# Optimization experiments

Measured on AMD Instinct MI355X. Metric: run time of the kernel, lower is better.

Reference implementation:

```python
import jax, jax.numpy as jnp
import numpy as np

N_EMBED = 1024
HEAD_SIZE = 128
B, T = 4, 4096

def setup_inputs() -> dict:
    key = jax.random.key(0)
    kx, kk, kq, kv = jax.random.split(key, 4)
    s = (1.0 / np.sqrt(N_EMBED)).astype(np.float32)
    return {
        "x": jax.random.normal(kx, (B, T, N_EMBED), dtype=jnp.float32),
        "W_key": jax.random.normal(kk, (N_EMBED, HEAD_SIZE), dtype=jnp.float32) * s,
        "W_query": jax.random.normal(kq, (N_EMBED, HEAD_SIZE), dtype=jnp.float32) * s,
        "W_value": jax.random.normal(kv, (N_EMBED, HEAD_SIZE), dtype=jnp.float32) * s,
    }

def reference(x, W_key, W_query, W_value):
    # x: [B,T,C]; single-head causal attention. NOTE: scale is C**-0.5 (n_embed),
    # matching the original source (not head_size**-0.5).
    Bn, Tn, C = x.shape
    k = jnp.einsum('btc,cd->btd', x, W_key)    # [B,T,d]
    q = jnp.einsum('btc,cd->btd', x, W_query)  # [B,T,d]
    v = jnp.einsum('btc,cd->btd', x, W_value)  # [B,T,d]
    scores = jnp.einsum('btd,bsd->bts', q, k) * (C ** -0.5)  # [B,T,T]
    causal = jnp.tril(jnp.ones((Tn, Tn), dtype=bool))
    scores = jnp.where(causal[None, :, :], scores, -jnp.inf)
    attn = jax.nn.softmax(scores, axis=-1)
    return jnp.einsum('bts,bsd->btd', attn, v)
```

## Files before the change

### kernel.cpp

```cpp
#include <hip/hip_runtime.h>
#include <hip/hip_bf16.h>

typedef __attribute__((ext_vector_type(8))) short bf16x8;
typedef __attribute__((ext_vector_type(4))) float f32x4;
typedef __attribute__((ext_vector_type(4))) unsigned short us4;

__device__ __forceinline__ unsigned short f2bf(float f) {
    union { float f; unsigned u; } c; c.f = f;
    unsigned u = c.u;
    u += 0x7fffu + ((u >> 16) & 1u);
    return (unsigned short)(u >> 16);
}
__device__ __forceinline__ float bf2f(unsigned short h) {
    union { unsigned u; float f; } c; c.u = ((unsigned)h) << 16;
    return c.f;
}
__device__ __forceinline__ unsigned cvt_pk_bf16(float lo, float hi) {
    unsigned r;
    asm volatile("v_cvt_pk_bf16_f32 %0, %1, %2" : "=v"(r) : "v"(lo), "v"(hi));
    return r;
}

#define QSCALE 0.04508422f

__global__ __launch_bounds__(256) void wconv_kernel(
        const float* __restrict__ Wk, const float* __restrict__ Wq,
        const float* __restrict__ Wv, unsigned short* __restrict__ WbT) {
    int idx = blockIdx.x * 256 + threadIdx.x;
    int n = idx >> 10, kk = idx & 1023;
    const float* W = (n < 128) ? Wk : (n < 256) ? Wq : Wv;
    int col = n & 127;
    WbT[idx] = f2bf(W[kk * 128 + col]);
}

__global__ __launch_bounds__(512) void qkv_gemm_kernel(
        const float* __restrict__ x, const unsigned short* __restrict__ WbT,
        unsigned short* __restrict__ kw, unsigned short* __restrict__ qw,
        unsigned short* __restrict__ vTw) {
    __shared__ __align__(16) unsigned short Al[32 * 72];
    __shared__ __align__(16) unsigned short Bl[384 * 72];
    const int tid = threadIdx.x;
    const int m0 = blockIdx.x * 32;
    const int w = tid >> 6, l = tid & 63;
    const int l15 = l & 15, lh = l >> 4;
    const int wr = w >> 2, wc = w & 3;

    f32x4 acc[6] = {};

    const int ar = tid >> 4, ac = (tid & 15) * 4;

    float4 aV;
    bf16x8 bV[6];

    auto issue = [&](int k0) {
        aV = *(const float4*)&x[(size_t)(m0 + ar) * 1024 + k0 + ac];
        for (int it = 0; it < 6; ++it) {
            int idx = it * 512 + tid;
            bV[it] = *(const bf16x8*)&WbT[(size_t)(idx >> 3) * 1024 + k0 + (idx & 7) * 8];
        }
    };

    issue(0);
    for (int t = 0; t < 16; ++t) {
        {
            uint2 p;
            p.x = cvt_pk_bf16(aV.x, aV.y);
            p.y = cvt_pk_bf16(aV.z, aV.w);
            *(uint2*)&Al[ar * 72 + ac] = p;
        }
        for (int it = 0; it < 6; ++it) {
            int idx = it * 512 + tid;
            *(bf16x8*)&Bl[(idx >> 3) * 72 + (idx & 7) * 8] = bV[it];
        }
        __syncthreads();
        if (t + 1 < 16) issue((t + 1) * 64);
        for (int kc = 0; kc < 2; ++kc) {
            bf16x8 a = *(bf16x8*)&Al[(wr * 16 + l15) * 72 + kc * 32 + lh * 8];
            for (int ni = 0; ni < 6; ++ni) {
                bf16x8 bb = *(bf16x8*)&Bl[(wc * 96 + ni * 16 + l15) * 72 + kc * 32 + lh * 8];
                acc[ni] = __builtin_amdgcn_mfma_f32_16x16x32_bf16(a, bb, acc[ni], 0, 0, 0);
            }
        }
        __syncthreads();
    }

    for (int ni = 0; ni < 6; ++ni) {
        int col = wc * 96 + ni * 16 + l15;
        int sect = col >> 7, cc = col & 127;
        if (sect < 2) {
            unsigned short* dst = (sect == 0) ? kw : qw;
            float fs = (sect == 0) ? 1.0f : QSCALE;
            for (int i = 0; i < 4; ++i) {
                int row = m0 + wr * 16 + lh * 4 + i;
                dst[(size_t)row * 128 + cc] = f2bf(acc[ni][i] * fs);
            }
        } else {
            int trow0 = m0 + wr * 16 + lh * 4;
            int b = trow0 >> 12, t0 = trow0 & 4095;
            union { unsigned short u[4]; us4 v; } pk;
            for (int i = 0; i < 4; ++i) pk.u[i] = f2bf(acc[ni][i]);
            *(us4*)&vTw[((size_t)(b * 128 + cc)) * 4096 + t0] = pk.v;
        }
    }
}

__global__ __launch_bounds__(512) void attn_kernel(
        const unsigned short* __restrict__ kw, const unsigned short* __restrict__ qw,
        const unsigned short* __restrict__ vTw,
        unsigned short* __restrict__ pO, float* __restrict__ pL,
        int nCPB, int G, int TPC) {
    __shared__ __align__(16) unsigned short Kl[64 * 128];
    __shared__ __align__(16) unsigned short Vl[128 * 64];
    __shared__ __align__(16) unsigned short Pl[8][1024];

    const int tid = threadIdx.x;
    const int wgid = blockIdx.x;
    const int xcd = wgid & 7, slot = wgid >> 3;
    const int b = xcd >> 1, half = xcd & 1;
    const int cid = (nCPB - 1) - (slot * 2 + half);
    const int halfG = G >> 1;
    int a = 0;
    while (halfG * (a + 1) * (a + 2) <= cid) ++a;
    int rem = cid - halfG * a * (a + 1);
    const int g = G * a + rem / (a + 1);
    const int c = rem % (a + 1);
    const int kt0 = c * TPC;
    const int kt1 = min(kt0 + TPC, 2 * g + 2);

    const int w = tid >> 6, l = tid & 63;
    const int l15 = l & 15, lh = l >> 4;
    const int qrow0 = g * 128 + w * 16;

    bf16x8 qa[4];
    {
        size_t grow = (size_t)b * 4096 + qrow0 + l15;
        for (int cc = 0; cc < 4; ++cc)
            qa[cc] = *(const bf16x8*)&qw[grow * 128 + cc * 32 + lh * 8];
    }
    bf16x8 ones;
    for (int u = 0; u < 8; ++u) ones[u] = (short)0x3F80;

    f32x4 o[8] = {};
    f32x4 lsa = {0.f, 0.f, 0.f, 0.f};

    const int kr_ = tid >> 3;
    const int vd_ = tid >> 2;
    bf16x8 kReg[2], vReg[2];
    auto issue = [&](int kt) {
        int kv0 = kt * 64;
        const unsigned short* ks = &kw[((size_t)(b * 4096 + kv0 + kr_)) * 128 + (tid & 7) * 16];
        kReg[0] = *(const bf16x8*)ks;
        kReg[1] = *(const bf16x8*)(ks + 8);
        const unsigned short* vs = &vTw[((size_t)(b * 128 + vd_)) * 4096 + kv0 + (tid & 3) * 16];
        vReg[0] = *(const bf16x8*)vs;
        vReg[1] = *(const bf16x8*)(vs + 8);
    };

    char* Plw = (char*)&Pl[w][0];

    issue(kt0);
    for (int kt = kt0; kt < kt1; ++kt) {
        __syncthreads();
        for (int it = 0; it < 2; ++it)
            *(bf16x8*)((char*)Kl + kr_ * 256 +
                    (((tid & 7) * 32 + it * 16) ^ ((kr_ & 7) << 4))) = kReg[it];
        for (int it = 0; it < 2; ++it)
            *(bf16x8*)((char*)Vl + vd_ * 128 +
                    (((tid & 3) * 32 + it * 16) ^ ((vd_ & 7) << 4))) = vReg[it];
        __syncthreads();
        if (kt + 1 < kt1) issue(kt + 1);

        const int kv0 = kt * 64;
        if (kv0 > qrow0 + 15) continue;

        f32x4 s[4];
        __builtin_amdgcn_s_setprio(1);
        for (int ni = 0; ni < 4; ++ni) {
            s[ni] = (f32x4){0.f, 0.f, 0.f, 0.f};
            int kr = ni * 16 + l15;
            int sw = (kr & 7) << 4;
            for (int cc = 0; cc < 4; ++cc) {
                bf16x8 bk = *(bf16x8*)((char*)Kl + kr * 256 + ((lh * 16 + cc * 64) ^ sw));
                s[ni] = __builtin_amdgcn_mfma_f32_16x16x32_bf16(bk, qa[cc], s[ni], 0, 0, 0);
            }
        }
        __builtin_amdgcn_s_setprio(0);

        if (kv0 + 63 > qrow0) {
            int qg = qrow0 + l15;
            for (int ni = 0; ni < 4; ++ni)
                for (int i = 0; i < 4; ++i)
                    if (kv0 + ni * 16 + lh * 4 + i > qg) s[ni][i] = -INFINITY;
        }
        for (int ni = 0; ni < 4; ++ni) {
            float p0 = exp2f(s[ni][0]), p1 = exp2f(s[ni][1]);
            float p2 = exp2f(s[ni][2]), p3 = exp2f(s[ni][3]);
            uint2 pk;
            pk.x = cvt_pk_bf16(p0, p1);
            pk.y = cvt_pk_bf16(p2, p3);
            *(uint2*)(Plw + l15 * 128 + ((ni * 32 + lh * 8) ^ ((l15 & 7) << 4))) = pk;
        }
        bf16x8 pa[2];
        for (int kc = 0; kc < 2; ++kc)
            pa[kc] = *(bf16x8*)(Plw + l15 * 128 +
                    ((kc * 64 + lh * 16) ^ ((l15 & 7) << 4)));
        __builtin_amdgcn_s_setprio(1);
        lsa = __builtin_amdgcn_mfma_f32_16x16x32_bf16(pa[1], ones,
              __builtin_amdgcn_mfma_f32_16x16x32_bf16(pa[0], ones, lsa, 0, 0, 0), 0, 0, 0);
        for (int nd = 0; nd < 8; ++nd) {
            int dr = nd * 16 + l15;
            int sw = (dr & 7) << 4;
            for (int kc = 0; kc < 2; ++kc) {
                bf16x8 bv = *(bf16x8*)((char*)Vl + dr * 128 + ((lh * 16 + kc * 64) ^ sw));
                o[nd] = __builtin_amdgcn_mfma_f32_16x16x32_bf16(pa[kc], bv, o[nd], 0, 0, 0);
            }
        }
        __builtin_amdgcn_s_setprio(0);
    }

    const int slot_ = b * nCPB + cid;
    unsigned short* po = pO + (size_t)slot_ * 16384;
    for (int nd = 0; nd < 8; ++nd)
        for (int i = 0; i < 4; ++i)
            po[(w * 16 + lh * 4 + i) * 128 + nd * 16 + l15] = f2bf(o[nd][i]);
    if (l15 == 0) {
        float* pl = pL + (size_t)slot_ * 128;
        for (int i = 0; i < 4; ++i)
            pl[w * 16 + lh * 4 + i] = lsa[i];
    }
}

__global__ __launch_bounds__(256) void combine_kernel(
        const unsigned short* __restrict__ pO, const float* __restrict__ pL,
        float* __restrict__ out, int nCPB, int G) {
    int idx = blockIdx.x * 256 + threadIdx.x;
    int row = idx >> 4, d8 = (idx & 15) * 8;
    int b = row >> 12, t = row & 4095;
    int g = t >> 7, rowin = t & 127;
    int a = g / G;
    int nch = a + 1;
    int base = b * nCPB + (G >> 1) * a * (a + 1) + (g - G * a) * (a + 1);

    float den = 0.f;
    float num[8] = {0.f, 0.f, 0.f, 0.f, 0.f, 0.f, 0.f, 0.f};
    for (int cc = 0; cc < nch; ++cc) {
        den += pL[(size_t)(base + cc) * 128 + rowin];
        bf16x8 ov = *(const bf16x8*)&pO[(size_t)(base + cc) * 16384 + rowin * 128 + d8];
        for (int u = 0; u < 8; ++u)
            num[u] += bf2f((unsigned short)ov[u]);
    }
    float inv = 1.f / den;
    for (int u = 0; u < 8; ++u)
        out[(size_t)row * 128 + d8 + u] = num[u] * inv;
}

extern "C" void kernel_launch(void* const* d_in, const int* in_sizes, int n_in,
                              void* d_out, int out_size, void* d_ws, size_t ws_size,
                              hipStream_t stream) {
    const float* x  = (const float*)d_in[0];
    const float* Wk = (const float*)d_in[1];
    const float* Wq = (const float*)d_in[2];
    const float* Wv = (const float*)d_in[3];
    float* out = (float*)d_out;

    char* ws = (char*)d_ws;
    unsigned short* WbT = (unsigned short*)(ws);
    unsigned short* kw  = (unsigned short*)(ws + 786432);
    unsigned short* qw  = (unsigned short*)(ws + 786432 + 4194304);
    unsigned short* vTw = (unsigned short*)(ws + 786432 + 2 * 4194304);
    size_t base = 786432 + 3 * (size_t)4194304;

    int nCPB, G, TPC;
    size_t need4 = base + (size_t)1088 * 32768 + (size_t)1088 * 512;
    if (ws_size >= need4) { nCPB = 272; G = 2; TPC = 4; }
    else                  { nCPB = 144; G = 4; TPC = 8; }
    int nslots = 4 * nCPB;
    unsigned short* pO = (unsigned short*)(ws + base);
    float*          pL = (float*)(ws + base + (size_t)nslots * 32768);

    wconv_kernel<<<1536, 256, 0, stream>>>(Wk, Wq, Wv, WbT);
    qkv_gemm_kernel<<<512, 512, 0, stream>>>(x, WbT, kw, qw, vTw);
    attn_kernel<<<nslots, 512, 0, stream>>>(kw, qw, vTw, pO, pL, nCPB, G, TPC);
    combine_kernel<<<1024, 256, 0, stream>>>(pO, pL, out, nCPB, G);
}
```

Baseline: 85.24 us.

## Enlarge QKV GEMM M-tile to 64 rows and double-buffer global prefetch

The QKV projection GEMM now handles 64 rows per block instead of 32, with each wave computing a 4x3 grid of MFMA tiles over all 64 rows and a 48-column strip. Weight tiles are therefore reused across twice as many rows, halving weight traffic. Two register sets of global loads alternate so the next-next k-step is prefetched. The grid shrinks from 512 to 256 blocks, which lowers occupancy and CU coverage and raises register pressure from the doubled prefetch buffers.

```diff
diff --git a/kernel.cpp b/kernel.cpp
--- a/kernel.cpp
+++ b/kernel.cpp
@@ -37,71 +37,108 @@
         const float* __restrict__ x, const unsigned short* __restrict__ WbT,
         unsigned short* __restrict__ kw, unsigned short* __restrict__ qw,
         unsigned short* __restrict__ vTw) {
-    __shared__ __align__(16) unsigned short Al[32 * 72];
+    __shared__ __align__(16) unsigned short Al[64 * 72];
     __shared__ __align__(16) unsigned short Bl[384 * 72];
     const int tid = threadIdx.x;
-    const int m0 = blockIdx.x * 32;
+    const int m0 = blockIdx.x * 64;
     const int w = tid >> 6, l = tid & 63;
     const int l15 = l & 15, lh = l >> 4;
-    const int wr = w >> 2, wc = w & 3;
-
-    f32x4 acc[6] = {};
-
-    const int ar = tid >> 4, ac = (tid & 15) * 4;
-
-    float4 aV;
-    bf16x8 bV[6];
-
-    auto issue = [&](int k0) {
-        aV = *(const float4*)&x[(size_t)(m0 + ar) * 1024 + k0 + ac];
-        for (int it = 0; it < 6; ++it) {
-            int idx = it * 512 + tid;
-            bV[it] = *(const bf16x8*)&WbT[(size_t)(idx >> 3) * 1024 + k0 + (idx & 7) * 8];
-        }
-    };
-
-    issue(0);
-    for (int t = 0; t < 16; ++t) {
-        {
-            uint2 p;
-            p.x = cvt_pk_bf16(aV.x, aV.y);
-            p.y = cvt_pk_bf16(aV.z, aV.w);
-            *(uint2*)&Al[ar * 72 + ac] = p;
-        }
-        for (int it = 0; it < 6; ++it) {
-            int idx = it * 512 + tid;
-            *(bf16x8*)&Bl[(idx >> 3) * 72 + (idx & 7) * 8] = bV[it];
-        }
-        __syncthreads();
-        if (t + 1 < 16) issue((t + 1) * 64);
-        for (int kc = 0; kc < 2; ++kc) {
-            bf16x8 a = *(bf16x8*)&Al[(wr * 16 + l15) * 72 + kc * 32 + lh * 8];
-            for (int ni = 0; ni < 6; ++ni) {
-                bf16x8 bb = *(bf16x8*)&Bl[(wc * 96 + ni * 16 + l15) * 72 + kc * 32 + lh * 8];
-                acc[ni] = __builtin_amdgcn_mfma_f32_16x16x32_bf16(a, bb, acc[ni], 0, 0, 0);
+
+    f32x4 acc[4][3] = {};
+
+    const int ar = tid >> 3, ac = (tid & 7) * 8;
+
+    float4 aA0, aA1, aB0, aB1;
+    bf16x8 bA0, bA1, bA2, bA3, bA4, bA5;
+    bf16x8 bB0, bB1, bB2, bB3, bB4, bB5;
+
+    const float* xr = &x[(size_t)(m0 + ar) * 1024 + ac];
+    const unsigned short* wr0 = &WbT[(size_t)((0 * 512 + tid) >> 3) * 1024 + ((0 * 512 + tid) & 7) * 8];
+    const unsigned short* wr1 = &WbT[(size_t)((1 * 512 + tid) >> 3) * 1024 + ((1 * 512 + tid) & 7) * 8];
+    const unsigned short* wr2 = &WbT[(size_t)((2 * 512 + tid) >> 3) * 1024 + ((2 * 512 + tid) & 7) * 8];
+    const unsigned short* wr3 = &WbT[(size_t)((3 * 512 + tid) >> 3) * 1024 + ((3 * 512 + tid) & 7) * 8];
+    const unsigned short* wr4 = &WbT[(size_t)((4 * 512 + tid) >> 3) * 1024 + ((4 * 512 + tid) & 7) * 8];
+    const unsigned short* wr5 = &WbT[(size_t)((5 * 512 + tid) >> 3) * 1024 + ((5 * 512 + tid) & 7) * 8];
+
+    #define ISSUE_A(k0) do { \
+        aA0 = *(const float4*)(xr + (k0)); aA1 = *(const float4*)(xr + (k0) + 4); \
+        bA0 = *(const bf16x8*)(wr0 + (k0)); bA1 = *(const bf16x8*)(wr1 + (k0)); \
+        bA2 = *(const bf16x8*)(wr2 + (k0)); bA3 = *(const bf16x8*)(wr3 + (k0)); \
+        bA4 = *(const bf16x8*)(wr4 + (k0)); bA5 = *(const bf16x8*)(wr5 + (k0)); } while (0)
+    #define ISSUE_B(k0) do { \
+        aB0 = *(const float4*)(xr + (k0)); aB1 = *(const float4*)(xr + (k0) + 4); \
+        bB0 = *(const bf16x8*)(wr0 + (k0)); bB1 = *(const bf16x8*)(wr1 + (k0)); \
+        bB2 = *(const bf16x8*)(wr2 + (k0)); bB3 = *(const bf16x8*)(wr3 + (k0)); \
+        bB4 = *(const bf16x8*)(wr4 + (k0)); bB5 = *(const bf16x8*)(wr5 + (k0)); } while (0)
+    #define WRITE_SET(a0, a1, b0, b1, b2, b3, b4, b5) do { \
+        us4 p; \
+        p.x = (unsigned short)(cvt_pk_bf16(a0.x, a0.y) & 0xffff); \
+        p.y = (unsigned short)(cvt_pk_bf16(a0.x, a0.y) >> 16); \
+        p.z = (unsigned short)(cvt_pk_bf16(a0.z, a0.w) & 0xffff); \
+        p.w = (unsigned short)(cvt_pk_bf16(a0.z, a0.w) >> 16); \
+        *(us4*)&Al[ar * 72 + ac] = p; \
+        p.x = (unsigned short)(cvt_pk_bf16(a1.x, a1.y) & 0xffff); \
+        p.y = (unsigned short)(cvt_pk_bf16(a1.x, a1.y) >> 16); \
+        p.z = (unsigned short)(cvt_pk_bf16(a1.z, a1.w) & 0xffff); \
+        p.w = (unsigned short)(cvt_pk_bf16(a1.z, a1.w) >> 16); \
+        *(us4*)&Al[ar * 72 + ac + 4] = p; \
+        *(bf16x8*)&Bl[((0 * 512 + tid) >> 3) * 72 + ((0 * 512 + tid) & 7) * 8] = b0; \
+        *(bf16x8*)&Bl[((1 * 512 + tid) >> 3) * 72 + ((1 * 512 + tid) & 7) * 8] = b1; \
+        *(bf16x8*)&Bl[((2 * 512 + tid) >> 3) * 72 + ((2 * 512 + tid) & 7) * 8] = b2; \
+        *(bf16x8*)&Bl[((3 * 512 + tid) >> 3) * 72 + ((3 * 512 + tid) & 7) * 8] = b3; \
+        *(bf16x8*)&Bl[((4 * 512 + tid) >> 3) * 72 + ((4 * 512 + tid) & 7) * 8] = b4; \
+        *(bf16x8*)&Bl[((5 * 512 + tid) >> 3) * 72 + ((5 * 512 + tid) & 7) * 8] = b5; } while (0)
+    #define MFMA_TILE() do { \
+        for (int kc = 0; kc < 2; ++kc) { \
+            bf16x8 a[4], bb[3]; \
+            for (int mi = 0; mi < 4; ++mi) \
+                a[mi] = *(bf16x8*)&Al[(mi * 16 + l15) * 72 + kc * 32 + lh * 8]; \
+            for (int ni = 0; ni < 3; ++ni) \
+                bb[ni] = *(bf16x8*)&Bl[(w * 48 + ni * 16 + l15) * 72 + kc * 32 + lh * 8]; \
+            for (int mi = 0; mi < 4; ++mi) \
+                for (int ni = 0; ni < 3; ++ni) \
+                    acc[mi][ni] = __builtin_amdgcn_mfma_f32_16x16x32_bf16( \
+                            a[mi], bb[ni], acc[mi][ni], 0, 0, 0); \
+        } } while (0)
+
+    ISSUE_A(0);
+    ISSUE_B(64);
+    for (int t = 0; t < 16; t += 2) {
+        WRITE_SET(aA0, aA1, bA0, bA1, bA2, bA3, bA4, bA5);
+        __syncthreads();
+        if (t + 2 < 16) ISSUE_A((t + 2) * 64);
+        MFMA_TILE();
+        __syncthreads();
+        WRITE_SET(aB0, aB1, bB0, bB1, bB2, bB3, bB4, bB5);
+        __syncthreads();
+        if (t + 3 < 16) ISSUE_B((t + 3) * 64);
+        MFMA_TILE();
+        __syncthreads();
+    }
+
+    for (int mi = 0; mi < 4; ++mi)
+        for (int ni = 0; ni < 3; ++ni) {
+            int col = w * 48 + ni * 16 + l15;
+            int sect = col >> 7, cc = col & 127;
+            if (sect < 2) {
+                unsigned short* dst = (sect == 0) ? kw : qw;
+                float fs = (sect == 0) ? 1.0f : QSCALE;
+                for (int i = 0; i < 4; ++i) {
+                    int row = m0 + mi * 16 + lh * 4 + i;
+                    dst[(size_t)row * 128 + cc] = f2bf(acc[mi][ni][i] * fs);
+                }
+            } else {
+                int trow0 = m0 + mi * 16 + lh * 4;
+                int b = trow0 >> 12, t0 = trow0 & 4095;
+                union { unsigned short u[4]; us4 v; } pk;
+                for (int i = 0; i < 4; ++i) pk.u[i] = f2bf(acc[ni == ni ? mi : mi][ni][i]);
+                *(us4*)&vTw[((size_t)(b * 128 + cc)) * 4096 + t0] = pk.v;
             }
         }
-        __syncthreads();
-    }
-
-    for (int ni = 0; ni < 6; ++ni) {
-        int col = wc * 96 + ni * 16 + l15;
-        int sect = col >> 7, cc = col & 127;
-        if (sect < 2) {
-            unsigned short* dst = (sect == 0) ? kw : qw;
-            float fs = (sect == 0) ? 1.0f : QSCALE;
-            for (int i = 0; i < 4; ++i) {
-                int row = m0 + wr * 16 + lh * 4 + i;
-                dst[(size_t)row * 128 + cc] = f2bf(acc[ni][i] * fs);
-            }
-        } else {
-            int trow0 = m0 + wr * 16 + lh * 4;
-            int b = trow0 >> 12, t0 = trow0 & 4095;
-            union { unsigned short u[4]; us4 v; } pk;
-            for (int i = 0; i < 4; ++i) pk.u[i] = f2bf(acc[ni][i]);
-            *(us4*)&vTw[((size_t)(b * 128 + cc)) * 4096 + t0] = pk.v;
-        }
-    }
+    #undef ISSUE_A
+    #undef ISSUE_B
+    #undef WRITE_SET
+    #undef MFMA_TILE
 }
 
 __global__ __launch_bounds__(512) void attn_kernel(
@@ -279,7 +316,7 @@
     float*          pL = (float*)(ws + base + (size_t)nslots * 32768);
 
     wconv_kernel<<<1536, 256, 0, stream>>>(Wk, Wq, Wv, WbT);
-    qkv_gemm_kernel<<<512, 512, 0, stream>>>(x, WbT, kw, qw, vTw);
+    qkv_gemm_kernel<<<256, 512, 0, stream>>>(x, WbT, kw, qw, vTw);
     attn_kernel<<<nslots, 512, 0, stream>>>(kw, qw, vTw, pO, pL, nCPB, G, TPC);
     combine_kernel<<<1024, 256, 0, stream>>>(pO, pL, out, nCPB, G);
 }
```

Result: faster. 77.68 us, median of 2 (-8.9%).

## Double-buffer QKV GEMM with direct global-to-LDS loads and larger M tiles

Applied to the files above, without the earlier changes.

Rewrites the QKV projection GEMM to use 64-row M tiles (256 blocks instead of 512), double-buffered LDS for both A and B, and global_load_lds to stream the bf16 weight tile straight into a XOR-swizzled LDS layout. Each wave now computes a 64x48 output block with 4x3 MFMA accumulators, reusing every A fragment across 3 B fragments and every B fragment across 4 A fragments. The goal is to overlap loading the next K slice with the current MFMAs, drop one barrier per iteration, and reduce repeated weight reads. The cost is more LDS and registers and half as many blocks, which may leave some CUs idle on this GPU.

```diff
diff --git a/kernel.cpp b/kernel.cpp
--- a/kernel.cpp
+++ b/kernel.cpp
@@ -19,6 +19,11 @@
     unsigned r;
     asm volatile("v_cvt_pk_bf16_f32 %0, %1, %2" : "=v"(r) : "v"(lo), "v"(hi));
     return r;
+}
+__device__ __forceinline__ void gload_lds16(const void* g, void* l) {
+    __builtin_amdgcn_global_load_lds(
+        (const __attribute__((address_space(1))) unsigned int*)g,
+        (__attribute__((address_space(3))) unsigned int*)l, 16, 0, 0);
 }
 
 #define QSCALE 0.04508422f
@@ -37,71 +42,96 @@
         const float* __restrict__ x, const unsigned short* __restrict__ WbT,
         unsigned short* __restrict__ kw, unsigned short* __restrict__ qw,
         unsigned short* __restrict__ vTw) {
-    __shared__ __align__(16) unsigned short Al[32 * 72];
-    __shared__ __align__(16) unsigned short Bl[384 * 72];
+    __shared__ __align__(16) unsigned short Bl[2][384 * 64];
+    __shared__ __align__(16) unsigned short Al[2][64 * 72];
     const int tid = threadIdx.x;
-    const int m0 = blockIdx.x * 32;
+    const int m0 = blockIdx.x * 64;
     const int w = tid >> 6, l = tid & 63;
     const int l15 = l & 15, lh = l >> 4;
-    const int wr = w >> 2, wc = w & 3;
-
-    f32x4 acc[6] = {};
-
-    const int ar = tid >> 4, ac = (tid & 15) * 4;
-
-    float4 aV;
-    bf16x8 bV[6];
-
-    auto issue = [&](int k0) {
-        aV = *(const float4*)&x[(size_t)(m0 + ar) * 1024 + k0 + ac];
-        for (int it = 0; it < 6; ++it) {
-            int idx = it * 512 + tid;
-            bV[it] = *(const bf16x8*)&WbT[(size_t)(idx >> 3) * 1024 + k0 + (idx & 7) * 8];
-        }
-    };
-
-    issue(0);
+
+    f32x4 acc[4][3] = {};
+
+    const int srcsw = ((((l & 7) * 16) ^ ((l >> 3) << 4)) >> 1);
+    const unsigned short* gB[6];
+    #pragma unroll
+    for (int it = 0; it < 6; ++it)
+        gB[it] = WbT + (size_t)(it * 64 + w * 8 + (l >> 3)) * 1024 + srcsw;
+
+    const float* xr = &x[(size_t)(m0 + (tid >> 3)) * 1024 + (tid & 7) * 8];
+    const int aoff = (tid >> 3) * 72 + (tid & 7) * 8;
+
+    #define STAGE_B(buf, k0) do { \
+        _Pragma("unroll") \
+        for (int it = 0; it < 6; ++it) \
+            gload_lds16(gB[it] + (k0), &Bl[buf][(it * 64 + w * 8) * 64]); \
+    } while (0)
+
+    STAGE_B(0, 0);
+    {
+        float4 a0 = *(const float4*)(xr);
+        float4 a1 = *(const float4*)(xr + 4);
+        uint4 pk;
+        pk.x = cvt_pk_bf16(a0.x, a0.y); pk.y = cvt_pk_bf16(a0.z, a0.w);
+        pk.z = cvt_pk_bf16(a1.x, a1.y); pk.w = cvt_pk_bf16(a1.z, a1.w);
+        *(uint4*)&Al[0][aoff] = pk;
+    }
+    __syncthreads();
+
+    int cur = 0;
     for (int t = 0; t < 16; ++t) {
-        {
-            uint2 p;
-            p.x = cvt_pk_bf16(aV.x, aV.y);
-            p.y = cvt_pk_bf16(aV.z, aV.w);
-            *(uint2*)&Al[ar * 72 + ac] = p;
-        }
-        for (int it = 0; it < 6; ++it) {
-            int idx = it * 512 + tid;
-            *(bf16x8*)&Bl[(idx >> 3) * 72 + (idx & 7) * 8] = bV[it];
+        float4 a0, a1;
+        const bool more = (t + 1 < 16);
+        if (more) {
+            STAGE_B(cur ^ 1, (t + 1) * 64);
+            a0 = *(const float4*)(xr + (t + 1) * 64);
+            a1 = *(const float4*)(xr + (t + 1) * 64 + 4);
+        }
+        const unsigned short* Bc = Bl[cur];
+        const unsigned short* Ac = Al[cur];
+        for (int kc = 0; kc < 2; ++kc) {
+            bf16x8 a[4], bb[3];
+            for (int mi = 0; mi < 4; ++mi)
+                a[mi] = *(const bf16x8*)&Ac[(mi * 16 + l15) * 72 + kc * 32 + lh * 8];
+            for (int ni = 0; ni < 3; ++ni) {
+                int n = w * 48 + ni * 16 + l15;
+                bb[ni] = *(const bf16x8*)((const char*)Bc + n * 128 +
+                        ((kc * 64 + lh * 16) ^ ((n & 7) << 4)));
+            }
+            for (int mi = 0; mi < 4; ++mi)
+                for (int ni = 0; ni < 3; ++ni)
+                    acc[mi][ni] = __builtin_amdgcn_mfma_f32_16x16x32_bf16(
+                            a[mi], bb[ni], acc[mi][ni], 0, 0, 0);
+        }
+        if (more) {
+            uint4 pk;
+            pk.x = cvt_pk_bf16(a0.x, a0.y); pk.y = cvt_pk_bf16(a0.z, a0.w);
+            pk.z = cvt_pk_bf16(a1.x, a1.y); pk.w = cvt_pk_bf16(a1.z, a1.w);
+            *(uint4*)&Al[cur ^ 1][aoff] = pk;
         }
         __syncthreads();
-        if (t + 1 < 16) issue((t + 1) * 64);
-        for (int kc = 0; kc < 2; ++kc) {
-            bf16x8 a = *(bf16x8*)&Al[(wr * 16 + l15) * 72 + kc * 32 + lh * 8];
-            for (int ni = 0; ni < 6; ++ni) {
-                bf16x8 bb = *(bf16x8*)&Bl[(wc * 96 + ni * 16 + l15) * 72 + kc * 32 + lh * 8];
-                acc[ni] = __builtin_amdgcn_mfma_f32_16x16x32_bf16(a, bb, acc[ni], 0, 0, 0);
+        cur ^= 1;
+    }
+    #undef STAGE_B
+
+    for (int mi = 0; mi < 4; ++mi)
+        for (int ni = 0; ni < 3; ++ni) {
+            int col = w * 48 + ni * 16 + l15;
+            int sect = col >> 7, cc = col & 127;
+            if (sect < 2) {
+                unsigned short* dst = (sect == 0) ? kw : qw;
+                float fs = (sect == 0) ? 1.0f : QSCALE;
+                for (int i = 0; i < 4; ++i) {
+                    int row = m0 + mi * 16 + lh * 4 + i;
+                    dst[(size_t)row * 128 + cc] = f2bf(acc[mi][ni][i] * fs);
+                }
+            } else {
+                int trow0 = m0 + mi * 16 + lh * 4;
+                int b = trow0 >> 12, t0 = trow0 & 4095;
+                union { unsigned short u[4]; us4 v; } pk;
+                for (int i = 0; i < 4; ++i) pk.u[i] = f2bf(acc[mi][ni][i]);
+                *(us4*)&vTw[((size_t)(b * 128 + cc)) * 4096 + t0] = pk.v;
             }
         }
-        __syncthreads();
-    }
-
-    for (int ni = 0; ni < 6; ++ni) {
-        int col = wc * 96 + ni * 16 + l15;
-        int sect = col >> 7, cc = col & 127;
-        if (sect < 2) {
-            unsigned short* dst = (sect == 0) ? kw : qw;
-            float fs = (sect == 0) ? 1.0f : QSCALE;
-            for (int i = 0; i < 4; ++i) {
-                int row = m0 + wr * 16 + lh * 4 + i;
-                dst[(size_t)row * 128 + cc] = f2bf(acc[ni][i] * fs);
-            }
-        } else {
-            int trow0 = m0 + wr * 16 + lh * 4;
-            int b = trow0 >> 12, t0 = trow0 & 4095;
-            union { unsigned short u[4]; us4 v; } pk;
-            for (int i = 0; i < 4; ++i) pk.u[i] = f2bf(acc[ni][i]);
-            *(us4*)&vTw[((size_t)(b * 128 + cc)) * 4096 + t0] = pk.v;
-        }
-    }
 }
 
 __global__ __launch_bounds__(512) void attn_kernel(
@@ -279,7 +309,7 @@
     float*          pL = (float*)(ws + base + (size_t)nslots * 32768);
 
     wconv_kernel<<<1536, 256, 0, stream>>>(Wk, Wq, Wv, WbT);
-    qkv_gemm_kernel<<<512, 512, 0, stream>>>(x, WbT, kw, qw, vTw);
+    qkv_gemm_kernel<<<256, 512, 0, stream>>>(x, WbT, kw, qw, vTw);
     attn_kernel<<<nslots, 512, 0, stream>>>(kw, qw, vTw, pO, pL, nCPB, G, TPC);
     combine_kernel<<<1024, 256, 0, stream>>>(pO, pL, out, nCPB, G);
 }
```

After: 81.36 us. 4.6% less time.
